# Kernel optimization log

Hardware: AMD Instinct MI355X
Metric: run time of the kernel (lower is better)

## Reference

```python
import jax, jax.numpy as jnp
import numpy as np

N, E, IN_CH, HID, HEADS, OUT = 50000, 400000, 256, 128, 4, 2
EPS = 1e-5

def _bn(x, g, b):
    # training-mode BatchNorm1d (biased variance), dropout treated as eval (off)
    m = jnp.mean(x, axis=0)
    v = jnp.mean((x - m) ** 2, axis=0)
    return (x - m) * jax.lax.rsqrt(v + EPS) * g + b

def _sage(x, src, dst, Wl, bl, Wr):
    # PyG SAGEConv: lin_l(mean_{j->i} x_j) + lin_r(x_i)
    msg = jax.ops.segment_sum(x[src], dst, num_segments=N)
    deg = jax.ops.segment_sum(jnp.ones((src.shape[0],), x.dtype), dst, num_segments=N)
    agg = msg / jnp.maximum(deg, 1.0)[:, None]
    return agg @ Wl.T + bl + x @ Wr.T

def _gat(x, src, dst, W, a_s, a_d, bias):
    # PyG GATConv with self-loops already appended to (src, dst); concat heads
    d = W.shape[0] // HEADS
    xh = (x @ W.T).reshape(N, HEADS, d)
    asrc = jnp.einsum('nhd,hd->nh', xh, a_s)
    adst = jnp.einsum('nhd,hd->nh', xh, a_d)
    e = jax.nn.leaky_relu(asrc[src] + adst[dst], 0.2)          # [E+N, H]
    m = jax.ops.segment_max(e, dst, num_segments=N)            # segment softmax
    ex = jnp.exp(e - m[dst])
    den = jax.ops.segment_sum(ex, dst, num_segments=N)
    alpha = ex / den[dst]
    out = jax.ops.segment_sum(alpha[:, :, None] * xh[src], dst, num_segments=N)
    return out.reshape(N, HEADS * d) + bias

def setup_inputs():
    key = jax.random.key(0)
    ks = jax.random.split(key, 12)
    rnd = lambda k, s: jax.random.normal(k, s, dtype=jnp.float32) * 0.05
    H4 = HID * HEADS
    return {
        'x': jax.random.normal(ks[0], (N, IN_CH), dtype=jnp.float32),
        'edge_index': jax.random.randint(ks[1], (2, E), 0, N, dtype=jnp.int32),
        'W1l': rnd(ks[2], (HID, IN_CH)), 'b1': jnp.zeros((HID,), jnp.float32),
        'W1r': rnd(ks[3], (HID, IN_CH)),
        'g1': jnp.ones((HID,), jnp.float32), 'be1': jnp.zeros((HID,), jnp.float32),
        'Wg': rnd(ks[4], (H4, HID)),
        'a_src': rnd(ks[5], (HEADS, HID)), 'a_dst': rnd(ks[6], (HEADS, HID)),
        'gbias': jnp.zeros((H4,), jnp.float32),
        'g2': jnp.ones((H4,), jnp.float32), 'be2': jnp.zeros((H4,), jnp.float32),
        'W2l': rnd(ks[7], (HID, H4)), 'b2': jnp.zeros((HID,), jnp.float32),
        'W2r': rnd(ks[8], (HID, H4)),
        'g3': jnp.ones((HID,), jnp.float32), 'be3': jnp.zeros((HID,), jnp.float32),
        'Wf1': rnd(ks[9], (HID // 2, HID)), 'bf1': jnp.zeros((HID // 2,), jnp.float32),
        'g4': jnp.ones((HID // 2,), jnp.float32), 'be4': jnp.zeros((HID // 2,), jnp.float32),
        'Wf2': rnd(ks[10], (OUT, HID // 2)), 'bf2': jnp.zeros((OUT,), jnp.float32),
    }

def reference(x, edge_index, W1l, b1, W1r, g1, be1, Wg, a_src, a_dst, gbias,
              g2, be2, W2l, b2, W2r, g3, be3, Wf1, bf1, g4, be4, Wf2, bf2):
    src, dst = edge_index[0], edge_index[1]
    h = jax.nn.elu(_bn(_sage(x, src, dst, W1l, b1, W1r), g1, be1))
    loop = jnp.arange(N, dtype=src.dtype)                      # GAT adds self-loops
    src_sl = jnp.concatenate([src, loop])
    dst_sl = jnp.concatenate([dst, loop])
    h = jax.nn.elu(_bn(_gat(h, src_sl, dst_sl, Wg, a_src, a_dst, gbias), g2, be2))
    h = jax.nn.elu(_bn(_sage(h, src, dst, W2l, b2, W2r), g3, be3))
    h = jax.nn.elu(_bn(h @ Wf1.T + bf1, g4, be4))
    return h @ Wf2.T + bf2
```

## Files before the change

### kernel.cpp

```cpp
#include <hip/hip_runtime.h>
#include <cstdint>
#include <cstddef>

#define NN 50000
#define EE 400000
#define BN_EPS 1e-5f
#define NB_SCAN 196
#define NWAVE 8192
#define GB 784
#define GAGG 2048
#define G2 64

typedef __attribute__((ext_vector_type(8))) short s16x8;
typedef __attribute__((ext_vector_type(4))) float floatx4;

__device__ __forceinline__ unsigned short f2b(float f) {
    uint32_t u = __float_as_uint(f);
    uint32_t r = (u + 0x7fffu + ((u >> 16) & 1u)) >> 16;
    return (unsigned short)r;
}
__device__ __forceinline__ uint32_t pack2(float a, float b) {
    return (uint32_t)f2b(a) | ((uint32_t)f2b(b) << 16);
}
__device__ __forceinline__ float b2f_lo(uint32_t u) { return __uint_as_float(u << 16); }
__device__ __forceinline__ float b2f_hi(uint32_t u) { return __uint_as_float(u & 0xffff0000u); }

#define GLD16(g, l) __builtin_amdgcn_global_load_lds(                          \
    (const __attribute__((address_space(1))) uint32_t*)(g),                    \
    (__attribute__((address_space(3))) uint32_t*)(l), 16, 0, 0)

__global__ __launch_bounds__(256)
void gemm_w256(const unsigned short* __restrict__ A,
               const unsigned short* __restrict__ W,
               unsigned short* __restrict__ Cb, float* __restrict__ Cf,
               int M, int K)
{
    __shared__ __align__(16) unsigned short As[128 * 32];
    __shared__ __align__(16) unsigned short Bs[256 * 32];
    const int t  = threadIdx.x;
    const int m0 = blockIdx.x * 128;
    const int lane = t & 63;
    const int lr = lane & 15;
    const int lq = lane >> 4;
    const int wid = t >> 6;
    const int wr  = (wid >> 1) * 64;
    const int wc2 = (wid & 1) * 128;

    floatx4 acc[4][8];
    const floatx4 zero = {0.f, 0.f, 0.f, 0.f};
    #pragma unroll
    for (int i = 0; i < 4; ++i)
        #pragma unroll
        for (int j = 0; j < 8; ++j) acc[i][j] = zero;

    for (int k0 = 0; k0 < K; k0 += 32) {
        #pragma unroll
        for (int it = 0; it < 2; ++it) {
            const int seg  = t + it * 256;
            const int row  = seg >> 2;
            const int klog = (seg & 3) ^ ((row >> 1) & 3);
            const unsigned short* ga = A + (size_t)min(m0 + row, M - 1) * K + k0 + klog * 8;
            GLD16(ga, As + seg * 8);
        }
        #pragma unroll
        for (int it = 0; it < 4; ++it) {
            const int seg  = t + it * 256;
            const int row  = seg >> 2;
            const int klog = (seg & 3) ^ ((row >> 1) & 3);
            const unsigned short* gb = W + (size_t)row * K + k0 + klog * 8;
            GLD16(gb, Bs + seg * 8);
        }
        __syncthreads();

        s16x8 af[4], bf[8];
        #pragma unroll
        for (int i = 0; i < 4; ++i) {
            const int ra = wr + i * 16 + lr;
            const int pa = lq ^ ((ra >> 1) & 3);
            af[i] = *(const s16x8*)(As + (ra * 4 + pa) * 8);
        }
        #pragma unroll
        for (int j = 0; j < 8; ++j) {
            const int rb = wc2 + j * 16 + lr;
            const int pb = lq ^ ((rb >> 1) & 3);
            bf[j] = *(const s16x8*)(Bs + (rb * 4 + pb) * 8);
        }
        #pragma unroll
        for (int i = 0; i < 4; ++i)
            #pragma unroll
            for (int j = 0; j < 8; ++j)
                acc[i][j] = __builtin_amdgcn_mfma_f32_16x16x32_bf16(
                    bf[j], af[i], acc[i][j], 0, 0, 0);
        __syncthreads();
    }

    const int orow = lane & 15;
    const int oc4  = (lane >> 4) * 4;
    #pragma unroll
    for (int i = 0; i < 4; ++i) {
        const int r = m0 + wr + i * 16 + orow;
        if (r >= M) continue;
        if (wc2 == 0) {
            #pragma unroll
            for (int j = 0; j < 8; ++j) {
                const int c = j * 16 + oc4;
                const floatx4 a = acc[i][j];
                uint2 ov;
                ov.x = pack2(a[0], a[1]);
                ov.y = pack2(a[2], a[3]);
                *(uint2*)(Cb + (size_t)r * 128 + c) = ov;
            }
        } else {
            #pragma unroll
            for (int j = 0; j < 8; ++j) {
                const int c = j * 16 + oc4;
                const floatx4 a = acc[i][j];
                *(float4*)(Cf + (size_t)r * 128 + c) = make_float4(a[0], a[1], a[2], a[3]);
            }
        }
    }
}

__global__ __launch_bounds__(256)
void gemm_bf16mm(const unsigned short* __restrict__ A,
                 const unsigned short* __restrict__ W,
                 const float* __restrict__ bias,
                 unsigned short* __restrict__ Cb, float* __restrict__ Cf,
                 int split, int M, int K, int Ncol, int ldb, int ldf)
{
    __shared__ __align__(16) unsigned short As[128 * 32];
    __shared__ __align__(16) unsigned short Bs[128 * 32];
    const int t  = threadIdx.x;
    const int m0 = blockIdx.y * 128;
    const int n0 = blockIdx.x * 128;
    const int lane = t & 63;
    const int lr = lane & 15;
    const int lq = lane >> 4;
    const int wr = (t >> 7) * 64;
    const int wc = ((t >> 6) & 1) * 64;

    floatx4 acc[4][4];
    const floatx4 zero = {0.f, 0.f, 0.f, 0.f};
    #pragma unroll
    for (int i = 0; i < 4; ++i)
        #pragma unroll
        for (int j = 0; j < 4; ++j) acc[i][j] = zero;

    for (int k0 = 0; k0 < K; k0 += 32) {
        #pragma unroll
        for (int it = 0; it < 2; ++it) {
            const int seg  = t + it * 256;
            const int row  = seg >> 2;
            const int klog = (seg & 3) ^ ((row >> 1) & 3);
            const unsigned short* ga = A + (size_t)min(m0 + row, M - 1) * K + k0 + klog * 8;
            GLD16(ga, As + seg * 8);
            const unsigned short* gb = W + (size_t)min(n0 + row, Ncol - 1) * K + k0 + klog * 8;
            GLD16(gb, Bs + seg * 8);
        }
        __syncthreads();

        s16x8 af[4], bf[4];
        #pragma unroll
        for (int i = 0; i < 4; ++i) {
            const int ra = wr + i * 16 + lr;
            const int pa = lq ^ ((ra >> 1) & 3);
            af[i] = *(const s16x8*)(As + (ra * 4 + pa) * 8);
            const int rb = wc + i * 16 + lr;
            const int pb = lq ^ ((rb >> 1) & 3);
            bf[i] = *(const s16x8*)(Bs + (rb * 4 + pb) * 8);
        }
        #pragma unroll
        for (int i = 0; i < 4; ++i)
            #pragma unroll
            for (int j = 0; j < 4; ++j)
                acc[i][j] = __builtin_amdgcn_mfma_f32_16x16x32_bf16(
                    bf[j], af[i], acc[i][j], 0, 0, 0);
        __syncthreads();
    }

    const int orow = lane & 15;
    const int oc4  = (lane >> 4) * 4;
    #pragma unroll
    for (int i = 0; i < 4; ++i) {
        const int r = m0 + wr + i * 16 + orow;
        if (r >= M) continue;
        #pragma unroll
        for (int j = 0; j < 4; ++j) {
            const int cb = n0 + wc + j * 16 + oc4;
            if (cb >= Ncol) continue;
            const floatx4 a = acc[i][j];
            if (cb < split) {
                uint2 ov;
                ov.x = pack2(a[0], a[1]);
                ov.y = pack2(a[2], a[3]);
                *(uint2*)(Cb + (size_t)r * ldb + cb) = ov;
            } else {
                const int cc = cb - split;
                float4 o = make_float4(a[0], a[1], a[2], a[3]);
                if (bias) {
                    o.x += bias[cc]; o.y += bias[cc + 1];
                    o.z += bias[cc + 2]; o.w += bias[cc + 3];
                }
                *(float4*)(Cf + (size_t)r * ldf + cc) = o;
            }
        }
    }
}

__global__ __launch_bounds__(256)
void gemm_heads(const unsigned short* __restrict__ agg,
                const unsigned short* __restrict__ Wg,
                const float* __restrict__ gbias,
                unsigned short* __restrict__ out)
{
    __shared__ __align__(16) unsigned short As[128 * 32];
    __shared__ __align__(16) unsigned short Bs[128 * 32];
    const int t  = threadIdx.x;
    const int m0 = blockIdx.x * 128;
    const int h  = blockIdx.y;
    const int lane = t & 63;
    const int lr = lane & 15;
    const int lq = lane >> 4;
    const int wr = (t >> 7) * 64;
    const int wc = ((t >> 6) & 1) * 64;

    floatx4 acc[4][4];
    const floatx4 zero = {0.f, 0.f, 0.f, 0.f};
    #pragma unroll
    for (int i = 0; i < 4; ++i)
        #pragma unroll
        for (int j = 0; j < 4; ++j) acc[i][j] = zero;

    for (int k0 = 0; k0 < 128; k0 += 32) {
        #pragma unroll
        for (int it = 0; it < 2; ++it) {
            const int seg  = t + it * 256;
            const int row  = seg >> 2;
            const int klog = (seg & 3) ^ ((row >> 1) & 3);
            const unsigned short* ga = agg + (size_t)min(m0 + row, NN - 1) * 512 + h * 128 + k0 + klog * 8;
            GLD16(ga, As + seg * 8);
            const unsigned short* gb = Wg + (size_t)(h * 128 + row) * 128 + k0 + klog * 8;
            GLD16(gb, Bs + seg * 8);
        }
        __syncthreads();

        s16x8 af[4], bf[4];
        #pragma unroll
        for (int i = 0; i < 4; ++i) {
            const int ra = wr + i * 16 + lr;
            const int pa = lq ^ ((ra >> 1) & 3);
            af[i] = *(const s16x8*)(As + (ra * 4 + pa) * 8);
            const int rb = wc + i * 16 + lr;
            const int pb = lq ^ ((rb >> 1) & 3);
            bf[i] = *(const s16x8*)(Bs + (rb * 4 + pb) * 8);
        }
        #pragma unroll
        for (int i = 0; i < 4; ++i)
            #pragma unroll
            for (int j = 0; j < 4; ++j)
                acc[i][j] = __builtin_amdgcn_mfma_f32_16x16x32_bf16(
                    bf[j], af[i], acc[i][j], 0, 0, 0);
        __syncthreads();
    }

    const int orow = lane & 15;
    const int oc4  = (lane >> 4) * 4;
    #pragma unroll
    for (int i = 0; i < 4; ++i) {
        const int r = m0 + wr + i * 16 + orow;
        if (r >= NN) continue;
        #pragma unroll
        for (int j = 0; j < 4; ++j) {
            const int c = wc + j * 16 + oc4;
            const floatx4 a = acc[i][j];
            const float* gb = gbias + h * 128 + c;
            uint2 ov;
            ov.x = pack2(a[0] + gb[0], a[1] + gb[1]);
            ov.y = pack2(a[2] + gb[2], a[3] + gb[3]);
            *(uint2*)(out + (size_t)r * 512 + h * 128 + c) = ov;
        }
    }
}

__global__ void k_conv_x(const float* __restrict__ x, unsigned short* __restrict__ xb)
{
    const int i8 = (blockIdx.x * 256 + threadIdx.x) * 8;
    const float4 f0 = *(const float4*)(x + i8);
    const float4 f1 = *(const float4*)(x + i8 + 4);
    uint4 o;
    o.x = pack2(f0.x, f0.y); o.y = pack2(f0.z, f0.w);
    o.z = pack2(f1.x, f1.y); o.w = pack2(f1.z, f1.w);
    *(uint4*)(xb + i8) = o;
}

__global__ void k_conv_w(const float* __restrict__ s0, const float* __restrict__ s1,
                         const float* __restrict__ s2, const float* __restrict__ s3,
                         const float* __restrict__ s4, const float* __restrict__ s5,
                         unsigned short* __restrict__ dst)
{
    const int i = blockIdx.x * 256 + threadIdx.x;
    if (i >= 270336) return;
    float v;
    if      (i < 32768)  v = s0[i];
    else if (i < 65536)  v = s1[i - 32768];
    else if (i < 131072) v = s2[i - 65536];
    else if (i < 196608) v = s3[i - 131072];
    else if (i < 262144) v = s4[i - 196608];
    else                 v = s5[i - 262144];
    dst[i] = f2b(v);
}

__global__ void k_atilde(const float* __restrict__ a_s, const float* __restrict__ a_d,
                         const float* __restrict__ Wg, float* __restrict__ ats,
                         float* __restrict__ atd)
{
    const int k = threadIdx.x;
    const int h = blockIdx.x;
    float s = 0.f, d = 0.f;
    for (int j = 0; j < 128; ++j) {
        const float w = Wg[(size_t)(h * 128 + j) * 128 + k];
        s += a_s[h * 128 + j] * w;
        d += a_d[h * 128 + j] * w;
    }
    ats[h * 128 + k] = s;
    atd[h * 128 + k] = d;
}

__global__ void k_count(const int* __restrict__ dst, int* __restrict__ cnt)
{
    int i = blockIdx.x * blockDim.x + threadIdx.x;
    if (i < EE) atomicAdd(&cnt[dst[i]], 1);
}

__global__ __launch_bounds__(256)
void k_scan_blk(const int* __restrict__ cnt, int* __restrict__ offs,
                int* __restrict__ bsum, int N)
{
    __shared__ int wsum[4];
    const int t = threadIdx.x;
    const int i = blockIdx.x * 256 + t;
    const int v = (i < N) ? cnt[i] : 0;
    int s = v;
    #pragma unroll
    for (int o = 1; o < 64; o <<= 1) {
        const int u = __shfl_up(s, o);
        if ((t & 63) >= o) s += u;
    }
    const int wid = t >> 6;
    if ((t & 63) == 63) wsum[wid] = s;
    __syncthreads();
    int base = 0;
    #pragma unroll
    for (int w = 0; w < 3; ++w) if (w < wid) base += wsum[w];
    if (i < N) offs[i] = base + s - v;
    if (t == 255) bsum[blockIdx.x] = base + s;
}

__global__ __launch_bounds__(256)
void k_scan_top(int* __restrict__ bsum, int* __restrict__ offs, int N)
{
    __shared__ int wsum[4];
    const int t = threadIdx.x;
    const int v = (t < NB_SCAN) ? bsum[t] : 0;
    int s = v;
    #pragma unroll
    for (int o = 1; o < 64; o <<= 1) {
        const int u = __shfl_up(s, o);
        if ((t & 63) >= o) s += u;
    }
    const int wid = t >> 6;
    if ((t & 63) == 63) wsum[wid] = s;
    __syncthreads();
    int base = 0;
    #pragma unroll
    for (int w = 0; w < 3; ++w) if (w < wid) base += wsum[w];
    if (t < NB_SCAN) bsum[t] = base + s - v;
    if (t == 255) offs[N] = base + s;
}

__global__ __launch_bounds__(256)
void k_scan_add(int* __restrict__ offs, const int* __restrict__ bsum, int N)
{
    const int i = blockIdx.x * 256 + threadIdx.x;
    if (i < N) offs[i] += bsum[blockIdx.x];
}

__global__ void k_fill(const int* __restrict__ src, const int* __restrict__ dst,
                       const int* __restrict__ offs, int* __restrict__ fill,
                       int* __restrict__ csr)
{
    int i = blockIdx.x * blockDim.x + threadIdx.x;
    if (i < EE) {
        int d = dst[i];
        int p = offs[d] + atomicAdd(&fill[d], 1);
        csr[p] = src[i];
    }
}

__global__ __launch_bounds__(256)
void k_sage_agg(const unsigned short* __restrict__ tl, float* __restrict__ tr,
                const float* __restrict__ bias, const int* __restrict__ offs,
                const int* __restrict__ csr, float* __restrict__ P)
{
    __shared__ float red[4][256];
    const int l  = threadIdx.x & 63;
    const int g  = l >> 4;
    const int c0 = (l & 15) * 8;
    const int wid = threadIdx.x >> 6;
    const int wv = blockIdx.x * 4 + wid;
    const float4 bv0 = *(const float4*)(bias + c0);
    const float4 bv1 = *(const float4*)(bias + c0 + 4);
    float ps[8] = {0.f,0.f,0.f,0.f,0.f,0.f,0.f,0.f};
    float qs[8] = {0.f,0.f,0.f,0.f,0.f,0.f,0.f,0.f};
    for (int nb = wv * 4; nb < NN; nb += NWAVE * 4) {
        const int n = nb + g;
        if (n < NN) {
            const int o0 = offs[n];
            const int o1 = offs[n + 1];
            const int deg = o1 - o0;
            float a[8] = {0.f,0.f,0.f,0.f,0.f,0.f,0.f,0.f};
            int j = o0;
            for (; j + 1 < o1; j += 2) {
                const int s0 = csr[j];
                const int s1 = csr[j + 1];
                const uint4 q0 = *(const uint4*)(tl + (size_t)s0 * 128 + c0);
                const uint4 q1 = *(const uint4*)(tl + (size_t)s1 * 128 + c0);
                a[0] += b2f_lo(q0.x); a[1] += b2f_hi(q0.x);
                a[2] += b2f_lo(q0.y); a[3] += b2f_hi(q0.y);
                a[4] += b2f_lo(q0.z); a[5] += b2f_hi(q0.z);
                a[6] += b2f_lo(q0.w); a[7] += b2f_hi(q0.w);
                a[0] += b2f_lo(q1.x); a[1] += b2f_hi(q1.x);
                a[2] += b2f_lo(q1.y); a[3] += b2f_hi(q1.y);
                a[4] += b2f_lo(q1.z); a[5] += b2f_hi(q1.z);
                a[6] += b2f_lo(q1.w); a[7] += b2f_hi(q1.w);
            }
            if (j < o1) {
                const int s0 = csr[j];
                const uint4 q0 = *(const uint4*)(tl + (size_t)s0 * 128 + c0);
                a[0] += b2f_lo(q0.x); a[1] += b2f_hi(q0.x);
                a[2] += b2f_lo(q0.y); a[3] += b2f_hi(q0.y);
                a[4] += b2f_lo(q0.z); a[5] += b2f_hi(q0.z);
                a[6] += b2f_lo(q0.w); a[7] += b2f_hi(q0.w);
            }
            const float inv = 1.f / fmaxf((float)deg, 1.f);
            float* tp = tr + (size_t)n * 128 + c0;
            float4 t0 = *(float4*)tp;
            float4 t1 = *(float4*)(tp + 4);
            float v[8];
            v[0] = t0.x + a[0] * inv + bv0.x; v[1] = t0.y + a[1] * inv + bv0.y;
            v[2] = t0.z + a[2] * inv + bv0.z; v[3] = t0.w + a[3] * inv + bv0.w;
            v[4] = t1.x + a[4] * inv + bv1.x; v[5] = t1.y + a[5] * inv + bv1.y;
            v[6] = t1.z + a[6] * inv + bv1.z; v[7] = t1.w + a[7] * inv + bv1.w;
            *(float4*)tp       = make_float4(v[0], v[1], v[2], v[3]);
            *(float4*)(tp + 4) = make_float4(v[4], v[5], v[6], v[7]);
            #pragma unroll
            for (int i = 0; i < 8; ++i) { ps[i] += v[i]; qs[i] += v[i] * v[i]; }
        }
    }
    #pragma unroll
    for (int i = 0; i < 8; ++i) {
        ps[i] += __shfl_xor(ps[i], 16); ps[i] += __shfl_xor(ps[i], 32);
        qs[i] += __shfl_xor(qs[i], 16); qs[i] += __shfl_xor(qs[i], 32);
    }
    if (l < 16) {
        #pragma unroll
        for (int i = 0; i < 8; ++i) {
            red[wid][c0 + i]       = ps[i];
            red[wid][128 + c0 + i] = qs[i];
        }
    }
    __syncthreads();
    const int tc = threadIdx.x;
    const float s = red[0][tc] + red[1][tc] + red[2][tc] + red[3][tc];
    P[(size_t)blockIdx.x * 256 + tc] = s;
}

__global__ __launch_bounds__(256)
void k_attn_agg(const unsigned short* __restrict__ h1, const float* __restrict__ asrc,
                const float* __restrict__ adst, const int* __restrict__ offs,
                const int* __restrict__ csr, unsigned short* __restrict__ agg)
{
    const int l  = threadIdx.x & 63;
    const int g  = l >> 4;
    const int c0 = (l & 15) * 8;
    const int wv = blockIdx.x * 4 + (threadIdx.x >> 6);
    for (int nb = wv * 4; nb < NN; nb += NWAVE * 4) {
        const int n = nb + g;
        if (n >= NN) continue;
        const int o0 = offs[n];
        const int deg = offs[n + 1] - o0;
        const int total = deg + 1;
        const float4 adv = *(const float4*)(adst + n * 4);
        float den0 = 0.f, den1 = 0.f, den2 = 0.f, den3 = 0.f;
        float acc[4][8];
        #pragma unroll
        for (int h = 0; h < 4; ++h)
            #pragma unroll
            for (int i = 0; i < 8; ++i) acc[h][i] = 0.f;
        int j = 0;
        for (; j + 1 < total; j += 2) {
            const int sidA = (j < deg) ? csr[o0 + j] : n;
            const int sidB = (j + 1 < deg) ? csr[o0 + j + 1] : n;
            const float4 avA = *(const float4*)(asrc + sidA * 4);
            const float4 avB = *(const float4*)(asrc + sidB * 4);
            const uint4 qA = *(const uint4*)(h1 + (size_t)sidA * 128 + c0);
            const uint4 qB = *(const uint4*)(h1 + (size_t)sidB * 128 + c0);
            float eA0 = avA.x + adv.x, eA1 = avA.y + adv.y;
            float eA2 = avA.z + adv.z, eA3 = avA.w + adv.w;
            eA0 = fmaxf(eA0, 0.2f * eA0); eA1 = fmaxf(eA1, 0.2f * eA1);
            eA2 = fmaxf(eA2, 0.2f * eA2); eA3 = fmaxf(eA3, 0.2f * eA3);
            const float wA0 = __expf(eA0), wA1 = __expf(eA1);
            const float wA2 = __expf(eA2), wA3 = __expf(eA3);
            float eB0 = avB.x + adv.x, eB1 = avB.y + adv.y;
            float eB2 = avB.z + adv.z, eB3 = avB.w + adv.w;
            eB0 = fmaxf(eB0, 0.2f * eB0); eB1 = fmaxf(eB1, 0.2f * eB1);
            eB2 = fmaxf(eB2, 0.2f * eB2); eB3 = fmaxf(eB3, 0.2f * eB3);
            const float wB0 = __expf(eB0), wB1 = __expf(eB1);
            const float wB2 = __expf(eB2), wB3 = __expf(eB3);
            den0 += wA0 + wB0; den1 += wA1 + wB1;
            den2 += wA2 + wB2; den3 += wA3 + wB3;
            float vA[8], vB[8];
            vA[0] = b2f_lo(qA.x); vA[1] = b2f_hi(qA.x);
            vA[2] = b2f_lo(qA.y); vA[3] = b2f_hi(qA.y);
            vA[4] = b2f_lo(qA.z); vA[5] = b2f_hi(qA.z);
            vA[6] = b2f_lo(qA.w); vA[7] = b2f_hi(qA.w);
            vB[0] = b2f_lo(qB.x); vB[1] = b2f_hi(qB.x);
            vB[2] = b2f_lo(qB.y); vB[3] = b2f_hi(qB.y);
            vB[4] = b2f_lo(qB.z); vB[5] = b2f_hi(qB.z);
            vB[6] = b2f_lo(qB.w); vB[7] = b2f_hi(qB.w);
            #pragma unroll
            for (int i = 0; i < 8; ++i) {
                acc[0][i] += wA0 * vA[i] + wB0 * vB[i];
                acc[1][i] += wA1 * vA[i] + wB1 * vB[i];
                acc[2][i] += wA2 * vA[i] + wB2 * vB[i];
                acc[3][i] += wA3 * vA[i] + wB3 * vB[i];
            }
        }
        if (j < total) {
            const int sid = (j < deg) ? csr[o0 + j] : n;
            const float4 av = *(const float4*)(asrc + sid * 4);
            const uint4 q = *(const uint4*)(h1 + (size_t)sid * 128 + c0);
            float e0 = av.x + adv.x, e1 = av.y + adv.y;
            float e2 = av.z + adv.z, e3 = av.w + adv.w;
            e0 = fmaxf(e0, 0.2f * e0); e1 = fmaxf(e1, 0.2f * e1);
            e2 = fmaxf(e2, 0.2f * e2); e3 = fmaxf(e3, 0.2f * e3);
            const float w0 = __expf(e0), w1 = __expf(e1);
            const float w2 = __expf(e2), w3 = __expf(e3);
            den0 += w0; den1 += w1; den2 += w2; den3 += w3;
            float v[8];
            v[0] = b2f_lo(q.x); v[1] = b2f_hi(q.x);
            v[2] = b2f_lo(q.y); v[3] = b2f_hi(q.y);
            v[4] = b2f_lo(q.z); v[5] = b2f_hi(q.z);
            v[6] = b2f_lo(q.w); v[7] = b2f_hi(q.w);
            #pragma unroll
            for (int i = 0; i < 8; ++i) {
                acc[0][i] += w0 * v[i];
                acc[1][i] += w1 * v[i];
                acc[2][i] += w2 * v[i];
                acc[3][i] += w3 * v[i];
            }
        }
        const float r[4] = {1.f / den0, 1.f / den1, 1.f / den2, 1.f / den3};
        #pragma unroll
        for (int h = 0; h < 4; ++h) {
            uint4 ov;
            ov.x = pack2(acc[h][0] * r[h], acc[h][1] * r[h]);
            ov.y = pack2(acc[h][2] * r[h], acc[h][3] * r[h]);
            ov.z = pack2(acc[h][4] * r[h], acc[h][5] * r[h]);
            ov.w = pack2(acc[h][6] * r[h], acc[h][7] * r[h]);
            *(uint4*)(agg + (size_t)n * 512 + h * 128 + c0) = ov;
        }
    }
}

__global__ __launch_bounds__(256)
void k_statsA_b2(const unsigned short* __restrict__ X, float* __restrict__ P)
{
    const int c = threadIdx.x * 2;
    const int b = blockIdx.x;
    const int r0 = b * 64;
    const int r1 = min(r0 + 64, NN);
    float s0 = 0.f, s1 = 0.f, q0 = 0.f, q1 = 0.f;
    for (int r = r0; r < r1; ++r) {
        const uint32_t u = *(const uint32_t*)(X + (size_t)r * 512 + c);
        const float v0 = b2f_lo(u), v1 = b2f_hi(u);
        s0 += v0; q0 += v0 * v0;
        s1 += v1; q1 += v1 * v1;
    }
    *(float2*)(P + (size_t)b * 1024 + c) = make_float2(s0, s1);
    *(float2*)(P + (size_t)b * 1024 + 512 + c) = make_float2(q0, q1);
}

__global__ __launch_bounds__(64)
void k_statsA_f(const float* __restrict__ X, float* __restrict__ P)
{
    const int c = threadIdx.x;
    const int b = blockIdx.x;
    const int r0 = b * 64;
    const int r1 = min(r0 + 64, NN);
    float s = 0.f, q = 0.f;
    for (int r = r0; r < r1; ++r) {
        const float v = X[(size_t)r * 64 + c];
        s += v; q += v * v;
    }
    P[(size_t)b * 128 + c] = s;
    P[(size_t)b * 128 + 64 + c] = q;
}

__global__ __launch_bounds__(256)
void k_red1(const float* __restrict__ P, float* __restrict__ P2, int C2, int nb)
{
    const int g = blockIdx.x;
    for (int c = threadIdx.x; c < C2; c += 256) {
        float s = 0.f;
        for (int b = g; b < nb; b += G2) s += P[(size_t)b * C2 + c];
        P2[(size_t)g * C2 + c] = s;
    }
}

template<int CHUNK>
__global__ void k_bn_reduce(const float* __restrict__ P, int C, int nb,
                            const float* __restrict__ g, const float* __restrict__ be,
                            float* __restrict__ scale, float* __restrict__ shift)
{
    __shared__ float sb[8 * CHUNK];
    __shared__ float qb[8 * CHUNK];
    const int t = threadIdx.x;
    const int cl = t & (CHUNK - 1);
    const int grp = t / CHUNK;
    const int c = blockIdx.x * CHUNK + cl;
    float s = 0.f, q = 0.f;
    for (int b = grp; b < nb; b += 8) {
        s += P[(size_t)b * 2 * C + c];
        q += P[(size_t)b * 2 * C + C + c];
    }
    sb[grp * CHUNK + cl] = s;
    qb[grp * CHUNK + cl] = q;
    __syncthreads();
    if (t < CHUNK) {
        float S = 0.f, Q = 0.f;
        #pragma unroll
        for (int g2 = 0; g2 < 8; ++g2) { S += sb[g2 * CHUNK + t]; Q += qb[g2 * CHUNK + t]; }
        const int cc = blockIdx.x * CHUNK + t;
        const float mean = S / (float)NN;
        float var = Q / (float)NN - mean * mean;
        var = fmaxf(var, 0.f);
        const float sc = g[cc] * rsqrtf(var + BN_EPS);
        scale[cc] = sc;
        shift[cc] = be[cc] - mean * sc;
    }
}

__global__ void k_bn_elu_f2b(const float* __restrict__ X, unsigned short* __restrict__ D,
                             const float* __restrict__ scale, const float* __restrict__ shift,
                             int Cm1, int total)
{
    const int i = (blockIdx.x * 256 + threadIdx.x) * 4;
    if (i >= total) return;
    const int c = i & Cm1;
    const float4 x = *(const float4*)(X + i);
    float o[4] = {x.x, x.y, x.z, x.w};
    #pragma unroll
    for (int k = 0; k < 4; ++k) {
        const float v = o[k] * scale[c + k] + shift[c + k];
        o[k] = (v > 0.f) ? v : (__expf(v) - 1.f);
    }
    uint2 ov;
    ov.x = pack2(o[0], o[1]); ov.y = pack2(o[2], o[3]);
    *(uint2*)(D + i) = ov;
}

__global__ void k_bn_elu_b2b(unsigned short* __restrict__ X,
                             const float* __restrict__ scale, const float* __restrict__ shift,
                             int Cm1, int total)
{
    const int i = (blockIdx.x * 256 + threadIdx.x) * 4;
    if (i >= total) return;
    const int c = i & Cm1;
    const uint2 u = *(const uint2*)(X + i);
    float o[4] = {b2f_lo(u.x), b2f_hi(u.x), b2f_lo(u.y), b2f_hi(u.y)};
    #pragma unroll
    for (int k = 0; k < 4; ++k) {
        const float v = o[k] * scale[c + k] + shift[c + k];
        o[k] = (v > 0.f) ? v : (__expf(v) - 1.f);
    }
    uint2 ov;
    ov.x = pack2(o[0], o[1]); ov.y = pack2(o[2], o[3]);
    *(uint2*)(X + i) = ov;
}

__global__ __launch_bounds__(256)
void k_bn_elu_coef(const float* __restrict__ X, unsigned short* __restrict__ D,
                   const float* __restrict__ scale, const float* __restrict__ shift,
                   const float* __restrict__ ats, const float* __restrict__ atd,
                   float* __restrict__ asrc, float* __restrict__ adst)
{
    const int l = threadIdx.x & 63;
    const int wv = blockIdx.x * 4 + (threadIdx.x >> 6);
    const int c = l * 2;
    const float2 sc = *(const float2*)(scale + c);
    const float2 sh = *(const float2*)(shift + c);
    float2 sa[4], da[4];
    #pragma unroll
    for (int h = 0; h < 4; ++h) {
        sa[h] = *(const float2*)(ats + h * 128 + c);
        da[h] = *(const float2*)(atd + h * 128 + c);
    }
    for (int n = wv; n < NN; n += NWAVE) {
        const float2 xv = *(const float2*)(X + (size_t)n * 128 + c);
        float v0 = xv.x * sc.x + sh.x;
        float v1 = xv.y * sc.y + sh.y;
        v0 = (v0 > 0.f) ? v0 : (__expf(v0) - 1.f);
        v1 = (v1 > 0.f) ? v1 : (__expf(v1) - 1.f);
        const uint32_t p = pack2(v0, v1);
        *(uint32_t*)(D + (size_t)n * 128 + c) = p;
        const float r0 = b2f_lo(p), r1 = b2f_hi(p);
        float ps[4], pd[4];
        #pragma unroll
        for (int h = 0; h < 4; ++h) {
            ps[h] = r0 * sa[h].x + r1 * sa[h].y;
            pd[h] = r0 * da[h].x + r1 * da[h].y;
        }
        #pragma unroll
        for (int o = 1; o < 64; o <<= 1) {
            #pragma unroll
            for (int h = 0; h < 4; ++h) {
                ps[h] += __shfl_xor(ps[h], o);
                pd[h] += __shfl_xor(pd[h], o);
            }
        }
        if (l == 0) {
            *(float4*)(asrc + n * 4) = make_float4(ps[0], ps[1], ps[2], ps[3]);
            *(float4*)(adst + n * 4) = make_float4(pd[0], pd[1], pd[2], pd[3]);
        }
    }
}

__global__ __launch_bounds__(256)
void k_bn_elu_fc2(const float* __restrict__ X, const float* __restrict__ scale,
                  const float* __restrict__ shift, const float* __restrict__ W,
                  const float* __restrict__ bias, float* __restrict__ out)
{
    const int c = threadIdx.x & 63;
    const int gw = blockIdx.x * 4 + (threadIdx.x >> 6);
    const float sc = scale[c], sh = shift[c];
    const float w0 = W[c], w1 = W[64 + c];
    const float b0 = bias[0], b1 = bias[1];
    for (int n = gw; n < NN; n += NWAVE) {
        float v = X[(size_t)n * 64 + c] * sc + sh;
        v = (v > 0.f) ? v : (__expf(v) - 1.f);
        float p0 = v * w0;
        float p1 = v * w1;
        #pragma unroll
        for (int o = 1; o < 64; o <<= 1) {
            p0 += __shfl_xor(p0, o);
            p1 += __shfl_xor(p1, o);
        }
        if (c == 0) {
            out[n * 2 + 0] = p0 + b0;
            out[n * 2 + 1] = p1 + b1;
        }
    }
}

extern "C" void kernel_launch(void* const* d_in, const int* in_sizes, int n_in,
                              void* d_out, int out_size, void* d_ws, size_t ws_size,
                              hipStream_t stream)
{
    const float* x     = (const float*)d_in[0];
    const int*   ei    = (const int*)d_in[1];
    const float* W1l   = (const float*)d_in[2];
    const float* b1    = (const float*)d_in[3];
    const float* W1r   = (const float*)d_in[4];
    const float* g1    = (const float*)d_in[5];
    const float* be1   = (const float*)d_in[6];
    const float* Wg    = (const float*)d_in[7];
    const float* a_s   = (const float*)d_in[8];
    const float* a_d   = (const float*)d_in[9];
    const float* gbias = (const float*)d_in[10];
    const float* g2    = (const float*)d_in[11];
    const float* be2   = (const float*)d_in[12];
    const float* W2l   = (const float*)d_in[13];
    const float* b2    = (const float*)d_in[14];
    const float* W2r   = (const float*)d_in[15];
    const float* g3    = (const float*)d_in[16];
    const float* be3   = (const float*)d_in[17];
    const float* Wf1   = (const float*)d_in[18];
    const float* bf1   = (const float*)d_in[19];
    const float* g4    = (const float*)d_in[20];
    const float* be4   = (const float*)d_in[21];
    const float* Wf2   = (const float*)d_in[22];
    const float* bf2   = (const float*)d_in[23];
    const int* src = ei;
    const int* dst = ei + EE;

    char* ws = (char*)d_ws;
    size_t off = 0;
    auto alloc = [&](size_t bytes) -> char* {
        char* p = ws + off;
        off += (bytes + 255) & ~(size_t)255;
        return p;
    };
    unsigned short* xb   = (unsigned short*)alloc((size_t)NN * 256 * 2);
    unsigned short* waren= (unsigned short*)alloc(270336 * 2);
    unsigned short* tlb  = (unsigned short*)alloc((size_t)NN * 128 * 2);
    float*          trF  = (float*)alloc((size_t)NN * 128 * 4);
    unsigned short* h1b  = (unsigned short*)alloc((size_t)NN * 128 * 2);
    unsigned short* aggb = (unsigned short*)alloc((size_t)NN * 512 * 2);
    unsigned short* gatb = (unsigned short*)alloc((size_t)NN * 512 * 2);
    float* asrc  = (float*)alloc((size_t)NN * 4 * 4);
    float* adst  = (float*)alloc((size_t)NN * 4 * 4);
    float* ats   = (float*)alloc(512 * 4);
    float* atd   = (float*)alloc(512 * 4);
    float* pstat = (float*)alloc((size_t)GB * 1024 * 4);
    float* pstat2= (float*)alloc((size_t)G2 * 1024 * 4);
    float* scsh  = (float*)alloc(1024 * 4);
    int*   cntfill = (int*)alloc((size_t)NN * 2 * 4);
    int*   offs  = (int*)alloc((size_t)(NN + 1) * 4);
    int*   csr   = (int*)alloc((size_t)EE * 4);
    int*   bsum  = (int*)alloc((size_t)NB_SCAN * 4);
    if (off > ws_size) return;
    (void)in_sizes; (void)n_in; (void)out_size;

    unsigned short* W1cat = waren;
    unsigned short* Wg_b  = waren + 65536;
    unsigned short* W2cat = waren + 131072;
    unsigned short* Wf1_b = waren + 262144;

    int* cnt  = cntfill;
    int* fill = cntfill + NN;
    float* scale = scsh;
    float* shift = scsh + 512;

    k_conv_x<<<6250, 256, 0, stream>>>(x, xb);
    k_conv_w<<<1056, 256, 0, stream>>>(W1l, W1r, Wg, W2l, W2r, Wf1, waren);
    k_atilde<<<4, 128, 0, stream>>>(a_s, a_d, Wg, ats, atd);
    hipMemsetAsync(cntfill, 0, (size_t)NN * 2 * 4, stream);
    k_count<<<(EE + 255) / 256, 256, 0, stream>>>(dst, cnt);
    k_scan_blk<<<NB_SCAN, 256, 0, stream>>>(cnt, offs, bsum, NN);
    k_scan_top<<<1, 256, 0, stream>>>(bsum, offs, NN);
    k_scan_add<<<NB_SCAN, 256, 0, stream>>>(offs, bsum, NN);
    k_fill<<<(EE + 255) / 256, 256, 0, stream>>>(src, dst, offs, fill, csr);

    const int gy = (NN + 127) / 128;

    gemm_w256<<<gy, 256, 0, stream>>>(xb, W1cat, tlb, trF, NN, 256);
    k_sage_agg<<<GAGG, 256, 0, stream>>>(tlb, trF, b1, offs, csr, pstat);
    k_red1<<<G2, 256, 0, stream>>>(pstat, pstat2, 256, GAGG);
    k_bn_reduce<128><<<1, 1024, 0, stream>>>(pstat2, 128, G2, g1, be1, scale, shift);
    k_bn_elu_coef<<<2048, 256, 0, stream>>>(trF, h1b, scale, shift, ats, atd, asrc, adst);

    k_attn_agg<<<2048, 256, 0, stream>>>(h1b, asrc, adst, offs, csr, aggb);
    gemm_heads<<<dim3(gy, 4), 256, 0, stream>>>(aggb, Wg_b, gbias, gatb);
    k_statsA_b2<<<GB, 256, 0, stream>>>(gatb, pstat);
    k_red1<<<G2, 256, 0, stream>>>(pstat, pstat2, 1024, GB);
    k_bn_reduce<128><<<4, 1024, 0, stream>>>(pstat2, 512, G2, g2, be2, scale, shift);
    k_bn_elu_b2b<<<(NN * 512 / 4 + 255) / 256, 256, 0, stream>>>(gatb, scale, shift, 511, NN * 512);

    gemm_w256<<<gy, 256, 0, stream>>>(gatb, W2cat, tlb, trF, NN, 512);
    k_sage_agg<<<GAGG, 256, 0, stream>>>(tlb, trF, b2, offs, csr, pstat);
    k_red1<<<G2, 256, 0, stream>>>(pstat, pstat2, 256, GAGG);
    k_bn_reduce<128><<<1, 1024, 0, stream>>>(pstat2, 128, G2, g3, be3, scale, shift);
    k_bn_elu_f2b<<<(NN * 128 / 4 + 255) / 256, 256, 0, stream>>>(trF, h1b, scale, shift, 127, NN * 128);

    gemm_bf16mm<<<dim3(1, gy), 256, 0, stream>>>(h1b, Wf1_b, bf1, nullptr, trF,
                                                 0, NN, 128, 64, 0, 64);
    k_statsA_f<<<GB, 64, 0, stream>>>(trF, pstat);
    k_red1<<<G2, 256, 0, stream>>>(pstat, pstat2, 128, GB);
    k_bn_reduce<64><<<1, 512, 0, stream>>>(pstat2, 64, G2, g4, be4, scale, shift);

    k_bn_elu_fc2<<<2048, 256, 0, stream>>>(trF, scale, shift, Wf2, bf2, (float*)d_out);
}
```

Measured before the change: 533.7 us.

## Sort nodes by in-degree for balanced aggregation and merge prep kernels

Adds a stable counting sort of nodes by clamped in-degree (local histogram, prefix, permutation kernels) and makes the SAGE and attention aggregation kernels iterate nodes through this permutation. The 4 nodes handled by one wave then have similar degree, which is meant to reduce divergence and load imbalance within a wave. It also merges the three input-conversion kernels into one launch. The cost is three extra small launches, a quadratic per-thread rank loop, and scattered node access order, which may hurt locality of per-node writes.

Result: no change. 539.3 us (+1.1%).

```diff
diff --git a/kernel.cpp b/kernel.cpp
--- a/kernel.cpp
+++ b/kernel.cpp
@@ -10,6 +10,8 @@
 #define GB 784
 #define GAGG 2048
 #define G2 64
+#define NBIN 64
+#define NB_SORT 196
 
 typedef __attribute__((ext_vector_type(8))) short s16x8;
 typedef __attribute__((ext_vector_type(4))) float floatx4;
@@ -282,48 +284,48 @@
     }
 }
 
-__global__ void k_conv_x(const float* __restrict__ x, unsigned short* __restrict__ xb)
-{
-    const int i8 = (blockIdx.x * 256 + threadIdx.x) * 8;
-    const float4 f0 = *(const float4*)(x + i8);
-    const float4 f1 = *(const float4*)(x + i8 + 4);
-    uint4 o;
-    o.x = pack2(f0.x, f0.y); o.y = pack2(f0.z, f0.w);
-    o.z = pack2(f1.x, f1.y); o.w = pack2(f1.z, f1.w);
-    *(uint4*)(xb + i8) = o;
-}
-
-__global__ void k_conv_w(const float* __restrict__ s0, const float* __restrict__ s1,
-                         const float* __restrict__ s2, const float* __restrict__ s3,
-                         const float* __restrict__ s4, const float* __restrict__ s5,
-                         unsigned short* __restrict__ dst)
-{
-    const int i = blockIdx.x * 256 + threadIdx.x;
-    if (i >= 270336) return;
-    float v;
-    if      (i < 32768)  v = s0[i];
-    else if (i < 65536)  v = s1[i - 32768];
-    else if (i < 131072) v = s2[i - 65536];
-    else if (i < 196608) v = s3[i - 131072];
-    else if (i < 262144) v = s4[i - 196608];
-    else                 v = s5[i - 262144];
-    dst[i] = f2b(v);
-}
-
-__global__ void k_atilde(const float* __restrict__ a_s, const float* __restrict__ a_d,
-                         const float* __restrict__ Wg, float* __restrict__ ats,
-                         float* __restrict__ atd)
-{
-    const int k = threadIdx.x;
-    const int h = blockIdx.x;
-    float s = 0.f, d = 0.f;
-    for (int j = 0; j < 128; ++j) {
-        const float w = Wg[(size_t)(h * 128 + j) * 128 + k];
-        s += a_s[h * 128 + j] * w;
-        d += a_d[h * 128 + j] * w;
-    }
-    ats[h * 128 + k] = s;
-    atd[h * 128 + k] = d;
+__global__ __launch_bounds__(256)
+void k_prep(const float* __restrict__ x, unsigned short* __restrict__ xb,
+            const float* __restrict__ s0, const float* __restrict__ s1,
+            const float* __restrict__ s2, const float* __restrict__ s3,
+            const float* __restrict__ s4, const float* __restrict__ s5,
+            unsigned short* __restrict__ wdst,
+            const float* __restrict__ a_s, const float* __restrict__ a_d,
+            float* __restrict__ ats, float* __restrict__ atd)
+{
+    const int b = blockIdx.x;
+    if (b < 6250) {
+        const int i8 = (b * 256 + threadIdx.x) * 8;
+        const float4 f0 = *(const float4*)(x + i8);
+        const float4 f1 = *(const float4*)(x + i8 + 4);
+        uint4 o;
+        o.x = pack2(f0.x, f0.y); o.y = pack2(f0.z, f0.w);
+        o.z = pack2(f1.x, f1.y); o.w = pack2(f1.z, f1.w);
+        *(uint4*)(xb + i8) = o;
+    } else if (b < 7306) {
+        const int i = (b - 6250) * 256 + threadIdx.x;
+        if (i >= 270336) return;
+        float v;
+        if      (i < 32768)  v = s0[i];
+        else if (i < 65536)  v = s1[i - 32768];
+        else if (i < 131072) v = s2[i - 65536];
+        else if (i < 196608) v = s3[i - 131072];
+        else if (i < 262144) v = s4[i - 196608];
+        else                 v = s5[i - 262144];
+        wdst[i] = f2b(v);
+    } else {
+        const int h = b - 7306;
+        const int k = threadIdx.x;
+        if (k >= 128) return;
+        float s = 0.f, d = 0.f;
+        for (int j = 0; j < 128; ++j) {
+            const float w = s2[(size_t)(h * 128 + j) * 128 + k];
+            s += a_s[h * 128 + j] * w;
+            d += a_d[h * 128 + j] * w;
+        }
+        ats[h * 128 + k] = s;
+        atd[h * 128 + k] = d;
+    }
 }
 
 __global__ void k_count(const int* __restrict__ dst, int* __restrict__ cnt)
@@ -398,9 +400,64 @@
 }
 
 __global__ __launch_bounds__(256)
+void k_lhist(const int* __restrict__ cnt, int* __restrict__ lhist)
+{
+    __shared__ int h[NBIN];
+    const int t = threadIdx.x;
+    if (t < NBIN) h[t] = 0;
+    __syncthreads();
+    const int n = blockIdx.x * 256 + t;
+    if (n < NN) atomicAdd(&h[min(cnt[n], NBIN - 1)], 1);
+    __syncthreads();
+    if (t < NBIN) lhist[blockIdx.x * NBIN + t] = h[t];
+}
+
+__global__ __launch_bounds__(64)
+void k_hsum(const int* __restrict__ lhist, int* __restrict__ loff,
+            int* __restrict__ gbase)
+{
+    __shared__ int tot[NBIN];
+    const int t = threadIdx.x;
+    int run = 0;
+    for (int b = 0; b < NB_SORT; ++b) {
+        loff[b * NBIN + t] = run;
+        run += lhist[b * NBIN + t];
+    }
+    tot[t] = run;
+    __syncthreads();
+    if (t == 0) {
+        int acc = 0;
+        for (int i = 0; i < NBIN; ++i) { const int v = tot[i]; gbase[i] = acc; acc += v; }
+    }
+}
+
+__global__ __launch_bounds__(256)
+void k_perm(const int* __restrict__ cnt, const int* __restrict__ loff,
+            const int* __restrict__ gbase, int* __restrict__ perm)
+{
+    __shared__ unsigned char bins[256];
+    const int t = threadIdx.x;
+    const int n = blockIdx.x * 256 + t;
+    int mybin = 255;
+    if (n < NN) {
+        mybin = min(cnt[n], NBIN - 1);
+        bins[t] = (unsigned char)mybin;
+    } else {
+        bins[t] = 255;
+    }
+    __syncthreads();
+    if (n < NN) {
+        int rank = 0;
+        for (int s = 0; s < t; ++s) rank += (bins[s] == (unsigned char)mybin);
+        perm[gbase[mybin] + loff[blockIdx.x * NBIN + mybin] + rank] = n;
+    }
+}
+
+__global__ __launch_bounds__(256)
 void k_sage_agg(const unsigned short* __restrict__ tl, float* __restrict__ tr,
                 const float* __restrict__ bias, const int* __restrict__ offs,
-                const int* __restrict__ csr, float* __restrict__ P)
+                const int* __restrict__ csr, const int* __restrict__ perm,
+                float* __restrict__ P)
 {
     __shared__ float red[4][256];
     const int l  = threadIdx.x & 63;
@@ -413,8 +470,9 @@
     float ps[8] = {0.f,0.f,0.f,0.f,0.f,0.f,0.f,0.f};
     float qs[8] = {0.f,0.f,0.f,0.f,0.f,0.f,0.f,0.f};
     for (int nb = wv * 4; nb < NN; nb += NWAVE * 4) {
-        const int n = nb + g;
-        if (n < NN) {
+        const int idx = nb + g;
+        if (idx < NN) {
+            const int n = perm[idx];
             const int o0 = offs[n];
             const int o1 = offs[n + 1];
             const int deg = o1 - o0;
@@ -478,15 +536,17 @@
 __global__ __launch_bounds__(256)
 void k_attn_agg(const unsigned short* __restrict__ h1, const float* __restrict__ asrc,
                 const float* __restrict__ adst, const int* __restrict__ offs,
-                const int* __restrict__ csr, unsigned short* __restrict__ agg)
+                const int* __restrict__ csr, const int* __restrict__ perm,
+                unsigned short* __restrict__ agg)
 {
     const int l  = threadIdx.x & 63;
     const int g  = l >> 4;
     const int c0 = (l & 15) * 8;
     const int wv = blockIdx.x * 4 + (threadIdx.x >> 6);
     for (int nb = wv * 4; nb < NN; nb += NWAVE * 4) {
-        const int n = nb + g;
-        if (n >= NN) continue;
+        const int idx = nb + g;
+        if (idx >= NN) continue;
+        const int n = perm[idx];
         const int o0 = offs[n];
         const int deg = offs[n + 1] - o0;
         const int total = deg + 1;
@@ -819,6 +879,10 @@
     int*   offs  = (int*)alloc((size_t)(NN + 1) * 4);
     int*   csr   = (int*)alloc((size_t)EE * 4);
     int*   bsum  = (int*)alloc((size_t)NB_SCAN * 4);
+    int*   lhist = (int*)alloc((size_t)NB_SORT * NBIN * 4);
+    int*   loff  = (int*)alloc((size_t)NB_SORT * NBIN * 4);
+    int*   gbase = (int*)alloc((size_t)NBIN * 4);
+    int*   perm  = (int*)alloc((size_t)NN * 4);
     if (off > ws_size) return;
     (void)in_sizes; (void)n_in; (void)out_size;
 
@@ -832,25 +896,27 @@
     float* scale = scsh;
     float* shift = scsh + 512;
 
-    k_conv_x<<<6250, 256, 0, stream>>>(x, xb);
-    k_conv_w<<<1056, 256, 0, stream>>>(W1l, W1r, Wg, W2l, W2r, Wf1, waren);
-    k_atilde<<<4, 128, 0, stream>>>(a_s, a_d, Wg, ats, atd);
+    k_prep<<<7310, 256, 0, stream>>>(x, xb, W1l, W1r, Wg, W2l, W2r, Wf1, waren,
+                                     a_s, a_d, ats, atd);
     hipMemsetAsync(cntfill, 0, (size_t)NN * 2 * 4, stream);
     k_count<<<(EE + 255) / 256, 256, 0, stream>>>(dst, cnt);
     k_scan_blk<<<NB_SCAN, 256, 0, stream>>>(cnt, offs, bsum, NN);
     k_scan_top<<<1, 256, 0, stream>>>(bsum, offs, NN);
     k_scan_add<<<NB_SCAN, 256, 0, stream>>>(offs, bsum, NN);
     k_fill<<<(EE + 255) / 256, 256, 0, stream>>>(src, dst, offs, fill, csr);
+    k_lhist<<<NB_SORT, 256, 0, stream>>>(cnt, lhist);
+    k_hsum<<<1, 64, 0, stream>>>(lhist, loff, gbase);
+    k_perm<<<NB_SORT, 256, 0, stream>>>(cnt, loff, gbase, perm);
 
     const int gy = (NN + 127) / 128;
 
     gemm_w256<<<gy, 256, 0, stream>>>(xb, W1cat, tlb, trF, NN, 256);
-    k_sage_agg<<<GAGG, 256, 0, stream>>>(tlb, trF, b1, offs, csr, pstat);
+    k_sage_agg<<<GAGG, 256, 0, stream>>>(tlb, trF, b1, offs, csr, perm, pstat);
     k_red1<<<G2, 256, 0, stream>>>(pstat, pstat2, 256, GAGG);
     k_bn_reduce<128><<<1, 1024, 0, stream>>>(pstat2, 128, G2, g1, be1, scale, shift);
     k_bn_elu_coef<<<2048, 256, 0, stream>>>(trF, h1b, scale, shift, ats, atd, asrc, adst);
 
-    k_attn_agg<<<2048, 256, 0, stream>>>(h1b, asrc, adst, offs, csr, aggb);
+    k_attn_agg<<<2048, 256, 0, stream>>>(h1b, asrc, adst, offs, csr, perm, aggb);
     gemm_heads<<<dim3(gy, 4), 256, 0, stream>>>(aggb, Wg_b, gbias, gatb);
     k_statsA_b2<<<GB, 256, 0, stream>>>(gatb, pstat);
     k_red1<<<G2, 256, 0, stream>>>(pstat, pstat2, 1024, GB);
@@ -858,7 +924,7 @@
     k_bn_elu_b2b<<<(NN * 512 / 4 + 255) / 256, 256, 0, stream>>>(gatb, scale, shift, 511, NN * 512);
 
     gemm_w256<<<gy, 256, 0, stream>>>(gatb, W2cat, tlb, trF, NN, 512);
-    k_sage_agg<<<GAGG, 256, 0, stream>>>(tlb, trF, b2, offs, csr, pstat);
+    k_sage_agg<<<GAGG, 256, 0, stream>>>(tlb, trF, b2, offs, csr, perm, pstat);
     k_red1<<<G2, 256, 0, stream>>>(pstat, pstat2, 256, GAGG);
     k_bn_reduce<128><<<1, 1024, 0, stream>>>(pstat2, 128, G2, g3, be3, scale, shift);
     k_bn_elu_f2b<<<(NN * 128 / 4 + 255) / 256, 256, 0, stream>>>(trF, h1b, scale, shift, 127, NN * 128);
```
